# Kernel optimization log

Hardware: AMD Instinct MI355X
Metric: run time of the kernel (lower is better)

The kernel has to match this reference:

```python
import jax, jax.numpy as jnp
import numpy as np


def setup_inputs() -> dict:
    key = jax.random.key(0)
    k1, k2, k3 = jax.random.split(key, 3)
    B, N, M, D = 4, 1024, 2048, 9
    outputs = jax.random.normal(k1, (B, N, D), dtype=jnp.float32)
    targets = jax.random.normal(k2, (B, M, D), dtype=jnp.float32)
    mask = jax.random.randint(k3, (B, M), 0, 2).astype(bool)
    return {"outputs": outputs, "targets": targets, "mask": mask, "k": 64, "max_pair": 1024}


def reference(outputs, targets, mask, k, max_pair):
    # outputs: (B, N, 9), targets: (B, M, 9), mask: (B, M) bool
    y_pred = outputs[:, :max_pair]
    B, N, D = y_pred.shape
    M = targets.shape[1]

    # Statistics over masked ground-truth rows (weighted, jit-friendly)
    w = mask.astype(y_pred.dtype)            # (B, M)
    S = w.sum()                               # number of valid rows
    mean = jnp.einsum('bm,bmd->d', w, targets) / S               # (9,)
    centered = (targets - mean) * w[..., None]                    # (B, M, 9)
    cov = jnp.einsum('bmd,bme->de', centered, centered) / (S - 1.0)
    cov_inv = jnp.linalg.pinv(cov)                                # (9, 9)

    def maha(x):
        # NOTE: original code subtracts the GT mean from the pairwise
        # differences before the quadratic form -- kept faithfully.
        xc = x - mean
        return jnp.einsum('...i,ij,...j->...', xc, cov_inv, xc)

    def topk_smallest_per_col(d, kk):
        # d: (R, N); torch.topk(dim=0, largest=False) -> smallest kk per column
        return -jax.lax.top_k(-d.T, kk)[0]    # (N, kk)

    # Intra loss: GT-vs-pred pairwise distances, masked rows only
    diff = targets[:, :, None, :] - y_pred[:, None, :, :]          # (B, M, N, 9)
    Dn = maha(diff)                                                 # (B, M, N)
    Dn = jnp.where(mask[:, :, None], Dn, jnp.inf).reshape(B * M, N)
    intra_loss = topk_smallest_per_col(Dn, k).mean()

    # Inter (regularization) loss: pred-vs-pred pairwise
    # y_reg1_expand[b,i,j] = y_pred[b,j]; y_reg2_expand[b,i,j] = y_pred[b,i]
    diff_r = y_pred[:, None, :, :] - y_pred[:, :, None, :]          # (B, N, N, 9)
    Dr = maha(diff_r).reshape(B * N, N)
    inter_loss = topk_smallest_per_col(Dr, k).mean()

    return intra_loss - 0.1 * inter_loss
```

## Files before the change

kernel.cpp:

```cpp
#include <hip/hip_runtime.h>
#include <math.h>

#define B_ 4
#define N_ 1024
#define M_ 2048
#define D_ 9
#define K_ 64
#define BM_ (B_*M_)
#define BN_ (B_*N_)
#define TPRE_STRIDE 12
#define PPRE_STRIDE 12
#define NPART 32
#define NSTAT 55
#define TSEL 512
#define BUD 128
#define NMRG 256

#define WS_A 0
#define WS_MEAN 81
#define WS_TPRE 96
#define WS_PPRE (WS_TPRE + BM_*TPRE_STRIDE)
#define WS_CS_INTRA (WS_PPRE + BN_*PPRE_STRIDE)
#define WS_CS_INTER (WS_CS_INTRA + N_)
#define WS_PART (WS_CS_INTER + N_)
#define WS_CANDI (WS_PART + NPART*(NSTAT+1))
#define WS_CANDE (WS_CANDI + 1024*2048)
#define WS_ACC (WS_CANDE + 1024*1024)

__device__ __forceinline__ unsigned f2key(float f) {
  unsigned b = __float_as_uint(f);
  return (b & 0x80000000u) ? ~b : (b | 0x80000000u);
}
__device__ __forceinline__ float key2f(unsigned k) {
  unsigned b = (k & 0x80000000u) ? (k ^ 0x80000000u) : ~k;
  return __uint_as_float(b);
}

__device__ int detect_mask_fmt(const void* mask, int* flags ) {
  int tid = threadIdx.x;
  if (tid < 2) flags[tid] = 0;
  __syncthreads();
  const unsigned char* mb = (const unsigned char*)mask;
  int la = 0, lb = 0;
  for (int i = tid; i < BM_; i += blockDim.x) {
    unsigned char c = mb[i];
    if (c) { if (i & 3) la = 1; else if ((i & 7) == 4) lb = 1; }
  }
  if (la) atomicOr(&flags[0], 1);
  if (lb) atomicOr(&flags[1], 1);
  __syncthreads();
  return flags[0] ? 0 : (flags[1] ? 1 : 2);
}
__device__ __forceinline__ int mask_at(const void* mask, int fmt, int t) {
  if (fmt == 0) return ((const unsigned char*)mask)[t] != 0;
  if (fmt == 1) return ((const int*)mask)[t] != 0;
  return ((const long long*)mask)[t] != 0LL;
}

__global__ __launch_bounds__(256) void stats_part_kernel(
    const float* __restrict__ targets, const void* __restrict__ mask,
    float* __restrict__ ws) {
  __shared__ int flags[2];
  __shared__ float wpart[4][NSTAT];
  int tid = threadIdx.x;
  int fmt = detect_mask_fmt(mask, flags);
  int t = blockIdx.x * 256 + tid;

  float v[NSTAT];
  float tv[D_];
  int m = mask_at(mask, fmt, t);
  const float* tp = targets + t * D_;
#pragma unroll
  for (int d = 0; d < D_; ++d) tv[d] = m ? tp[d] : 0.f;
  v[0] = m ? 1.f : 0.f;
#pragma unroll
  for (int d = 0; d < D_; ++d) v[1 + d] = tv[d];
  {
    int p = 10;
#pragma unroll
    for (int i = 0; i < D_; ++i)
#pragma unroll
      for (int j = i; j < D_; ++j, ++p) v[p] = tv[i] * tv[j];
  }
#pragma unroll
  for (int off = 32; off > 0; off >>= 1)
#pragma unroll
    for (int p = 0; p < NSTAT; ++p) v[p] += __shfl_down(v[p], off);
  int wave = tid >> 6, lane = tid & 63;
  if (lane == 0)
#pragma unroll
    for (int p = 0; p < NSTAT; ++p) wpart[wave][p] = v[p];
  __syncthreads();
  if (tid < NSTAT) {
    float s = wpart[0][tid] + wpart[1][tid] + wpart[2][tid] + wpart[3][tid];
    ws[WS_PART + blockIdx.x * (NSTAT + 1) + tid] = s;
  }
}

__global__ __launch_bounds__(256) void pre_kernel(
    const float* __restrict__ outputs, const float* __restrict__ targets,
    const void* __restrict__ mask, float* __restrict__ ws) {
  __shared__ int flags[2];
  __shared__ float tot[NSTAT];
  __shared__ float Atmp[9][9];
  __shared__ float Ash[81];
  __shared__ float msh[D_];
  int tid = threadIdx.x;
  int fmt = detect_mask_fmt(mask, flags);
  if (blockIdx.x == 0 && tid == 0) {
    long long* acc = (long long*)(ws + WS_ACC);
    acc[0] = 0; acc[1] = 0; acc[2] = 0;
  }
  if (tid < NSTAT) {
    double s = 0.0;
    for (int b = 0; b < NPART; ++b)
      s += (double)ws[WS_PART + b * (NSTAT + 1) + tid];
    tot[tid] = (float)s;
  }
  __syncthreads();
  if (tid < 64) {
    int lane = tid;
    float S = tot[0];
    float col[9];
    int j = lane - 9;
    if (lane < 9) {
      float mj = tot[1 + lane] / S;
#pragma unroll
      for (int r = 0; r < 9; ++r) {
        float mr = tot[1 + r] / S;
        int i0 = r < lane ? r : lane;
        int j0 = r < lane ? lane : r;
        int p = i0 * 9 - (i0 * (i0 - 1)) / 2 + (j0 - i0);
        col[r] = (tot[10 + p] - S * mr * mj) / (S - 1.0f);
      }
    } else {
#pragma unroll
      for (int r = 0; r < 9; ++r) col[r] = (r == j) ? 1.f : 0.f;
    }
#pragma unroll
    for (int c = 0; c < 9; ++c) {
      float pv = __shfl(col[c], c);
      float inv = 1.f / pv;
      col[c] *= inv;
      float f[9];
#pragma unroll
      for (int r = 0; r < 9; ++r) f[r] = __shfl(col[r], c);
#pragma unroll
      for (int r = 0; r < 9; ++r)
        if (r != c) col[r] -= f[r] * col[c];
    }
    if (lane >= 9 && lane < 18) {
#pragma unroll
      for (int r = 0; r < 9; ++r) Atmp[r][j] = col[r];
    }
  }
  __syncthreads();
  if (tid < 9) msh[tid] = tot[1 + tid] / tot[0];
  for (int idx = tid; idx < 81; idx += 256) {
    int i0 = idx / 9, j0 = idx % 9;
    Ash[idx] = 0.5f * (Atmp[i0][j0] + Atmp[j0][i0]);
  }
  __syncthreads();

  int idx = blockIdx.x * 256 + tid;
  if (idx < BM_) {
    const float* tp = targets + idx * D_;
    float u[D_];
#pragma unroll
    for (int d = 0; d < D_; ++d) u[d] = tp[d] - msh[d];
    float cu = 0.f; float au[D_];
#pragma unroll
    for (int i = 0; i < D_; ++i) {
      float s = 0.f;
#pragma unroll
      for (int j = 0; j < D_; ++j) s += Ash[i * D_ + j] * u[j];
      au[i] = s; cu += u[i] * s;
    }
    if (!mask_at(mask, fmt, idx)) cu = INFINITY;
    float* o = ws + WS_TPRE + idx * TPRE_STRIDE;
#pragma unroll
    for (int d = 0; d < D_; ++d) o[d] = au[d];
    o[9] = cu; o[10] = 0.f; o[11] = 0.f;
  } else if (idx < BM_ + BN_) {
    int r = idx - BM_;
    const float* yp = outputs + r * D_;
    float y[D_], q[D_], aq[D_];
#pragma unroll
    for (int d = 0; d < D_; ++d) { y[d] = yp[d]; q[d] = y[d] + msh[d]; }
    float cp = 0.f, cq = 0.f;
#pragma unroll
    for (int i = 0; i < D_; ++i) {
      float sy = 0.f, sq = 0.f;
#pragma unroll
      for (int j = 0; j < D_; ++j) {
        sy += Ash[i * D_ + j] * y[j];
        sq += Ash[i * D_ + j] * q[j];
      }
      cp += y[i] * sy;
      aq[i] = sq; cq += q[i] * sq;
    }
    float* o = ws + WS_PPRE + r * PPRE_STRIDE;
#pragma unroll
    for (int d = 0; d < D_; ++d) o[d] = aq[d];
    o[9] = cq; o[10] = cp; o[11] = 0.f;
  }
}

template <int PER>
__device__ __forceinline__ unsigned bisect64(const unsigned* key) {
  unsigned kmin = 0xFFFFFFFFu;
#pragma unroll
  for (int j = 0; j < PER; ++j) kmin = key[j] < kmin ? key[j] : kmin;
  unsigned gmin = kmin, mmax = kmin;
#pragma unroll
  for (int off = 32; off > 0; off >>= 1) {
    unsigned a = (unsigned)__shfl_xor((int)gmin, off);
    unsigned b = (unsigned)__shfl_xor((int)mmax, off);
    gmin = a < gmin ? a : gmin;
    mmax = b > mmax ? b : mmax;
  }
  unsigned lo = gmin, hi = mmax;
  while (lo < hi) {
    unsigned mid = lo + ((hi - lo) >> 1);
    int cnt = 0;
#pragma unroll
    for (int j = 0; j < PER; ++j) cnt += __popcll(__ballot(key[j] <= mid));
    if (cnt >= K_) hi = mid; else lo = mid + 1;
  }
  return lo;
}

template <int PER>
__device__ __forceinline__ void sel_thresh2(const unsigned* k0,
                                            const unsigned* k1,
                                            unsigned& T0o, unsigned& T1o,
                                            int& st0, int& st1) {
  unsigned mn0 = 0xFFFFFFFFu, mn1 = 0xFFFFFFFFu;
#pragma unroll
  for (int j = 0; j < PER; ++j) {
    mn0 = k0[j] < mn0 ? k0[j] : mn0;
    mn1 = k1[j] < mn1 ? k1[j] : mn1;
  }
  unsigned g0 = mn0, x0 = mn0, g1 = mn1, x1 = mn1;
#pragma unroll
  for (int off = 32; off > 0; off >>= 1) {
    unsigned a0 = (unsigned)__shfl_xor((int)g0, off);
    unsigned b0 = (unsigned)__shfl_xor((int)x0, off);
    unsigned a1 = (unsigned)__shfl_xor((int)g1, off);
    unsigned b1 = (unsigned)__shfl_xor((int)x1, off);
    g0 = a0 < g0 ? a0 : g0;  x0 = b0 > x0 ? b0 : x0;
    g1 = a1 < g1 ? a1 : g1;  x1 = b1 > x1 ? b1 : x1;
  }
  unsigned lo0 = g0, hi0 = x0, lo1 = g1, hi1 = x1;
  int c0 = 0, c1 = 0;
#pragma unroll
  for (int j = 0; j < PER; ++j) {
    c0 += __popcll(__ballot(k0[j] <= hi0));
    c1 += __popcll(__ballot(k1[j] <= hi1));
  }
  while (((lo0 < hi0) && (c0 > BUD)) || ((lo1 < hi1) && (c1 > BUD))) {
    int a0 = (lo0 < hi0) && (c0 > BUD);
    int a1 = (lo1 < hi1) && (c1 > BUD);
    unsigned mid0 = lo0 + ((hi0 - lo0) >> 1);
    unsigned mid1 = lo1 + ((hi1 - lo1) >> 1);
    int n0 = 0, n1 = 0;
#pragma unroll
    for (int j = 0; j < PER; ++j) {
      n0 += __popcll(__ballot(k0[j] <= mid0));
      n1 += __popcll(__ballot(k1[j] <= mid1));
    }
    if (a0) { if (n0 >= K_) { hi0 = mid0; c0 = n0; } else lo0 = mid0 + 1; }
    if (a1) { if (n1 >= K_) { hi1 = mid1; c1 = n1; } else lo1 = mid1 + 1; }
  }
  T0o = hi0; st0 = (c0 > BUD);
  T1o = hi1; st1 = (c1 > BUD);
}

template <int PER>
__device__ __forceinline__ void compactB(const unsigned* key, unsigned T,
                                         int strict, float* candw, int lane) {
  unsigned long long lmask = (1ull << lane) - 1ull;
  int n = 0;
#pragma unroll
  for (int j = 0; j < PER; ++j) {
    bool p = strict ? (key[j] < T) : (key[j] <= T);
    unsigned long long m = __ballot(p);
    if (p) candw[n + __popcll(m & lmask)] = key2f(key[j]);
    n += __popcll(m);
  }
  float tv = key2f(T);
  for (int i = n + lane; i < BUD; i += 64) candw[i] = tv;
}

template <int NP>
__device__ __forceinline__ float final_sum(const float* __restrict__ cand,
                                           int lane) {
  unsigned kk[NP];
#pragma unroll
  for (int j = 0; j < NP; ++j) kk[j] = f2key(cand[j * 64 + lane]);
  unsigned T = bisect64<NP>(kk);
  float s = 0.f; int c = 0;
#pragma unroll
  for (int j = 0; j < NP; ++j)
    if (kk[j] < T) { s += key2f(kk[j]); c++; }
#pragma unroll
  for (int off = 32; off > 0; off >>= 1) {
    s += __shfl_down(s, off);
    c += __shfl_down(c, off);
  }
  return s + (float)(K_ - c) * key2f(T);
}

__global__ __launch_bounds__(TSEL) void select_kernel(
    const float* __restrict__ outputs, const float* __restrict__ wsro,
    float* __restrict__ ws) {
  __shared__ float vsh[2][B_][D_];
  __shared__ float cvsh[2][B_];
  int tid = threadIdx.x, wave = tid >> 6, lane = tid & 63;
  int bid = blockIdx.x;
  int is_intra = bid < N_;
  int p = is_intra ? (bid >> 1) : (bid - N_);
  int h = is_intra ? (bid & 1) : 0;
  int c0 = 2 * p;
  if (tid < 2 * B_ * D_) {
    int c = tid / (B_ * D_), rem = tid % (B_ * D_), b = rem / D_, d = rem % D_;
    vsh[c][b][d] = outputs[(b * N_ + c0 + c) * D_ + d];
  }
  if (tid < 2 * B_) {
    int c = tid >> 2, b = tid & 3;
    cvsh[c][b] = wsro[WS_PPRE + (b * N_ + c0 + c) * PPRE_STRIDE + 10];
  }
  __syncthreads();
  constexpr int PER = 8;
  unsigned k0[PER], k1[PER];
  if (is_intra) {
    const float* pre = wsro + WS_TPRE;
    int rowbase = h * 4096;
#pragma unroll
    for (int bbb = 0; bbb < 2; ++bbb) {
      int b = 2 * h + bbb;
      float v0[D_], v1[D_];
#pragma unroll
      for (int d = 0; d < D_; ++d) { v0[d] = vsh[0][b][d]; v1[d] = vsh[1][b][d]; }
      float cv0 = cvsh[0][b], cv1 = cvsh[1][b];
#pragma unroll
      for (int jj = 0; jj < 4; ++jj) {
        int j = bbb * 4 + jj;
        const float* row = pre + (rowbase + tid + TSEL * j) * TPRE_STRIDE;
        float4 a0 = *(const float4*)row;
        float4 a1 = *(const float4*)(row + 4);
        float2 a2 = *(const float2*)(row + 8);
        float d0 = a0.x * v0[0] + a0.y * v0[1] + a0.z * v0[2] + a0.w * v0[3] +
                   a1.x * v0[4] + a1.y * v0[5] + a1.z * v0[6] + a1.w * v0[7] +
                   a2.x * v0[8];
        float d1 = a0.x * v1[0] + a0.y * v1[1] + a0.z * v1[2] + a0.w * v1[3] +
                   a1.x * v1[4] + a1.y * v1[5] + a1.z * v1[6] + a1.w * v1[7] +
                   a2.x * v1[8];
        k0[j] = f2key(a2.y + cv0 - 2.0f * d0);
        k1[j] = f2key(a2.y + cv1 - 2.0f * d1);
      }
      __builtin_amdgcn_sched_barrier(0);
    }
  } else {
    const float* pre = wsro + WS_PPRE;
#pragma unroll
    for (int bb = 0; bb < B_; ++bb) {
      float v0[D_], v1[D_];
#pragma unroll
      for (int d = 0; d < D_; ++d) { v0[d] = vsh[0][bb][d]; v1[d] = vsh[1][bb][d]; }
      float cv0 = cvsh[0][bb], cv1 = cvsh[1][bb];
#pragma unroll
      for (int jj = 0; jj < 2; ++jj) {
        int j = bb * 2 + jj;
        const float* row = pre + (tid + TSEL * j) * PPRE_STRIDE;
        float4 a0 = *(const float4*)row;
        float4 a1 = *(const float4*)(row + 4);
        float2 a2 = *(const float2*)(row + 8);
        float d0 = a0.x * v0[0] + a0.y * v0[1] + a0.z * v0[2] + a0.w * v0[3] +
                   a1.x * v0[4] + a1.y * v0[5] + a1.z * v0[6] + a1.w * v0[7] +
                   a2.x * v0[8];
        float d1 = a0.x * v1[0] + a0.y * v1[1] + a0.z * v1[2] + a0.w * v1[3] +
                   a1.x * v1[4] + a1.y * v1[5] + a1.z * v1[6] + a1.w * v1[7] +
                   a2.x * v1[8];
        k0[j] = f2key(a2.y + cv0 - 2.0f * d0);
        k1[j] = f2key(a2.y + cv1 - 2.0f * d1);
      }
      __builtin_amdgcn_sched_barrier(0);
    }
  }
  unsigned T0, T1; int st0, st1;
  sel_thresh2<PER>(k0, k1, T0, T1, st0, st1);
  if (is_intra) {
    compactB<PER>(k0, T0, st0,
                  ws + WS_CANDI + (c0) * 2048 + h * 1024 + wave * BUD, lane);
    compactB<PER>(k1, T1, st1,
                  ws + WS_CANDI + (c0 + 1) * 2048 + h * 1024 + wave * BUD, lane);
  } else {
    compactB<PER>(k0, T0, st0,
                  ws + WS_CANDE + (c0) * 1024 + wave * BUD, lane);
    compactB<PER>(k1, T1, st1,
                  ws + WS_CANDE + (c0 + 1) * 1024 + wave * BUD, lane);
  }
}

__global__ __launch_bounds__(512) void merge_kernel(
    const float* __restrict__ wsro, float* __restrict__ ws,
    float* __restrict__ out) {
  __shared__ long long part[8];
  int wave = threadIdx.x >> 6, lane = threadIdx.x & 63;
  int gw = blockIdx.x * 8 + wave;
  unsigned long long* acc = (unsigned long long*)(ws + WS_ACC);
  float s;
  int is_intra = gw < N_;
  if (is_intra) s = final_sum<32>(wsro + WS_CANDI + gw * 2048, lane);
  else          s = final_sum<16>(wsro + WS_CANDE + (gw - N_) * 1024, lane);
  if (lane == 0) part[wave] = (long long)llrint((double)s * 4294967296.0);
  __syncthreads();
  if (threadIdx.x == 0) {
    long long t = 0;
#pragma unroll
    for (int w = 0; w < 8; ++w) t += part[w];
    atomicAdd(&acc[is_intra ? 0 : 1], (unsigned long long)t);
    __threadfence();
    unsigned long long old = atomicAdd(&acc[2], 1ull);
    if (old == (unsigned long long)(NMRG - 1)) {
      long long aI = (long long)atomicAdd(&acc[0], 0ull);
      long long aE = (long long)atomicAdd(&acc[1], 0ull);
      double dn = 4294967296.0 * (double)N_ * (double)K_;
      out[0] = (float)((double)aI / dn - 0.1 * ((double)aE / dn));
    }
  }
}

extern "C" void kernel_launch(void* const* d_in, const int* in_sizes, int n_in,
                              void* d_out, int out_size, void* d_ws,
                              size_t ws_size, hipStream_t stream) {
  const float* outputs = (const float*)d_in[0];
  const float* targets = (const float*)d_in[1];
  const void* mask = d_in[2];
  float* ws = (float*)d_ws;

  hipLaunchKernelGGL(stats_part_kernel, dim3(NPART), dim3(256), 0, stream,
                     targets, mask, ws);
  hipLaunchKernelGGL(pre_kernel, dim3((BM_ + BN_ + 255) / 256), dim3(256), 0,
                     stream, outputs, targets, mask, ws);
  hipLaunchKernelGGL(select_kernel, dim3(N_ + N_ / 2), dim3(TSEL), 0, stream,
                     outputs, ws, ws);
  hipLaunchKernelGGL(merge_kernel, dim3(NMRG), dim3(512), 0, stream,
                     ws, ws, (float*)d_out);
}
```

Baseline: 76.78 us.

## Fold stats reduction into pre kernel and store candidates as sort keys

Removes the separate stats_part_kernel launch. Every pre_kernel block now redundantly computes the full masked mean and covariance sums over all 8192 target rows with a strided per-thread loop, so the partial-sum workspace and one dependent launch go away. Candidate buffers now store the ordered unsigned keys directly, which avoids key/float conversions in the compaction and merge steps. The cost is that each of the 48 pre blocks reads all targets and does about 32 loop iterations of the 55-term accumulation, which lengthens each block. The reduction also switches from double to float.

```diff
diff --git a/kernel.cpp b/kernel.cpp
--- a/kernel.cpp
+++ b/kernel.cpp
@@ -10,20 +10,14 @@
 #define BN_ (B_*N_)
 #define TPRE_STRIDE 12
 #define PPRE_STRIDE 12
-#define NPART 32
 #define NSTAT 55
 #define TSEL 512
 #define BUD 128
 #define NMRG 256
 
-#define WS_A 0
-#define WS_MEAN 81
 #define WS_TPRE 96
 #define WS_PPRE (WS_TPRE + BM_*TPRE_STRIDE)
-#define WS_CS_INTRA (WS_PPRE + BN_*PPRE_STRIDE)
-#define WS_CS_INTER (WS_CS_INTRA + N_)
-#define WS_PART (WS_CS_INTER + N_)
-#define WS_CANDI (WS_PART + NPART*(NSTAT+1))
+#define WS_CANDI (WS_PPRE + BN_*PPRE_STRIDE)
 #define WS_CANDE (WS_CANDI + 1024*2048)
 #define WS_ACC (WS_CANDE + 1024*1024)
 
@@ -57,50 +51,11 @@
   return ((const long long*)mask)[t] != 0LL;
 }
 
-__global__ __launch_bounds__(256) void stats_part_kernel(
-    const float* __restrict__ targets, const void* __restrict__ mask,
-    float* __restrict__ ws) {
-  __shared__ int flags[2];
-  __shared__ float wpart[4][NSTAT];
-  int tid = threadIdx.x;
-  int fmt = detect_mask_fmt(mask, flags);
-  int t = blockIdx.x * 256 + tid;
-
-  float v[NSTAT];
-  float tv[D_];
-  int m = mask_at(mask, fmt, t);
-  const float* tp = targets + t * D_;
-#pragma unroll
-  for (int d = 0; d < D_; ++d) tv[d] = m ? tp[d] : 0.f;
-  v[0] = m ? 1.f : 0.f;
-#pragma unroll
-  for (int d = 0; d < D_; ++d) v[1 + d] = tv[d];
-  {
-    int p = 10;
-#pragma unroll
-    for (int i = 0; i < D_; ++i)
-#pragma unroll
-      for (int j = i; j < D_; ++j, ++p) v[p] = tv[i] * tv[j];
-  }
-#pragma unroll
-  for (int off = 32; off > 0; off >>= 1)
-#pragma unroll
-    for (int p = 0; p < NSTAT; ++p) v[p] += __shfl_down(v[p], off);
-  int wave = tid >> 6, lane = tid & 63;
-  if (lane == 0)
-#pragma unroll
-    for (int p = 0; p < NSTAT; ++p) wpart[wave][p] = v[p];
-  __syncthreads();
-  if (tid < NSTAT) {
-    float s = wpart[0][tid] + wpart[1][tid] + wpart[2][tid] + wpart[3][tid];
-    ws[WS_PART + blockIdx.x * (NSTAT + 1) + tid] = s;
-  }
-}
-
 __global__ __launch_bounds__(256) void pre_kernel(
     const float* __restrict__ outputs, const float* __restrict__ targets,
     const void* __restrict__ mask, float* __restrict__ ws) {
   __shared__ int flags[2];
+  __shared__ float wpart[4][NSTAT];
   __shared__ float tot[NSTAT];
   __shared__ float Atmp[9][9];
   __shared__ float Ash[81];
@@ -111,12 +66,38 @@
     long long* acc = (long long*)(ws + WS_ACC);
     acc[0] = 0; acc[1] = 0; acc[2] = 0;
   }
-  if (tid < NSTAT) {
-    double s = 0.0;
-    for (int b = 0; b < NPART; ++b)
-      s += (double)ws[WS_PART + b * (NSTAT + 1) + tid];
-    tot[tid] = (float)s;
-  }
+  {
+    float v[NSTAT];
+#pragma unroll
+    for (int p = 0; p < NSTAT; ++p) v[p] = 0.f;
+    for (int it = 0; it < 32; ++it) {
+      int t = it * 256 + tid;
+      int m = mask_at(mask, fmt, t);
+      const float* tp = targets + t * D_;
+      float tv[D_];
+#pragma unroll
+      for (int d = 0; d < D_; ++d) tv[d] = m ? tp[d] : 0.f;
+      v[0] += m ? 1.f : 0.f;
+#pragma unroll
+      for (int d = 0; d < D_; ++d) v[1 + d] += tv[d];
+      int p = 10;
+#pragma unroll
+      for (int i = 0; i < D_; ++i)
+#pragma unroll
+        for (int j = i; j < D_; ++j, ++p) v[p] += tv[i] * tv[j];
+    }
+#pragma unroll
+    for (int off = 32; off > 0; off >>= 1)
+#pragma unroll
+      for (int p = 0; p < NSTAT; ++p) v[p] += __shfl_down(v[p], off);
+    int wave = tid >> 6, lane = tid & 63;
+    if (lane == 0)
+#pragma unroll
+      for (int p = 0; p < NSTAT; ++p) wpart[wave][p] = v[p];
+  }
+  __syncthreads();
+  if (tid < NSTAT)
+    tot[tid] = wpart[0][tid] + wpart[1][tid] + wpart[2][tid] + wpart[3][tid];
   __syncthreads();
   if (tid < 64) {
     int lane = tid;
@@ -278,26 +259,25 @@
 
 template <int PER>
 __device__ __forceinline__ void compactB(const unsigned* key, unsigned T,
-                                         int strict, float* candw, int lane) {
+                                         int strict, unsigned* candw, int lane) {
   unsigned long long lmask = (1ull << lane) - 1ull;
   int n = 0;
 #pragma unroll
   for (int j = 0; j < PER; ++j) {
     bool p = strict ? (key[j] < T) : (key[j] <= T);
     unsigned long long m = __ballot(p);
-    if (p) candw[n + __popcll(m & lmask)] = key2f(key[j]);
+    if (p) candw[n + __popcll(m & lmask)] = key[j];
     n += __popcll(m);
   }
-  float tv = key2f(T);
-  for (int i = n + lane; i < BUD; i += 64) candw[i] = tv;
+  for (int i = n + lane; i < BUD; i += 64) candw[i] = T;
 }
 
 template <int NP>
-__device__ __forceinline__ float final_sum(const float* __restrict__ cand,
+__device__ __forceinline__ float final_sum(const unsigned* __restrict__ cand,
                                            int lane) {
   unsigned kk[NP];
 #pragma unroll
-  for (int j = 0; j < NP; ++j) kk[j] = f2key(cand[j * 64 + lane]);
+  for (int j = 0; j < NP; ++j) kk[j] = cand[j * 64 + lane];
   unsigned T = bisect64<NP>(kk);
   float s = 0.f; int c = 0;
 #pragma unroll
@@ -390,16 +370,14 @@
   }
   unsigned T0, T1; int st0, st1;
   sel_thresh2<PER>(k0, k1, T0, T1, st0, st1);
+  unsigned* candi = (unsigned*)(ws + WS_CANDI);
+  unsigned* cande = (unsigned*)(ws + WS_CANDE);
   if (is_intra) {
-    compactB<PER>(k0, T0, st0,
-                  ws + WS_CANDI + (c0) * 2048 + h * 1024 + wave * BUD, lane);
-    compactB<PER>(k1, T1, st1,
-                  ws + WS_CANDI + (c0 + 1) * 2048 + h * 1024 + wave * BUD, lane);
+    compactB<PER>(k0, T0, st0, candi + (c0) * 2048 + h * 1024 + wave * BUD, lane);
+    compactB<PER>(k1, T1, st1, candi + (c0 + 1) * 2048 + h * 1024 + wave * BUD, lane);
   } else {
-    compactB<PER>(k0, T0, st0,
-                  ws + WS_CANDE + (c0) * 1024 + wave * BUD, lane);
-    compactB<PER>(k1, T1, st1,
-                  ws + WS_CANDE + (c0 + 1) * 1024 + wave * BUD, lane);
+    compactB<PER>(k0, T0, st0, cande + (c0) * 1024 + wave * BUD, lane);
+    compactB<PER>(k1, T1, st1, cande + (c0 + 1) * 1024 + wave * BUD, lane);
   }
 }
 
@@ -412,8 +390,10 @@
   unsigned long long* acc = (unsigned long long*)(ws + WS_ACC);
   float s;
   int is_intra = gw < N_;
-  if (is_intra) s = final_sum<32>(wsro + WS_CANDI + gw * 2048, lane);
-  else          s = final_sum<16>(wsro + WS_CANDE + (gw - N_) * 1024, lane);
+  if (is_intra)
+    s = final_sum<32>((const unsigned*)(wsro + WS_CANDI) + gw * 2048, lane);
+  else
+    s = final_sum<16>((const unsigned*)(wsro + WS_CANDE) + (gw - N_) * 1024, lane);
   if (lane == 0) part[wave] = (long long)llrint((double)s * 4294967296.0);
   __syncthreads();
   if (threadIdx.x == 0) {
@@ -440,8 +420,6 @@
   const void* mask = d_in[2];
   float* ws = (float*)d_ws;
 
-  hipLaunchKernelGGL(stats_part_kernel, dim3(NPART), dim3(256), 0, stream,
-                     targets, mask, ws);
   hipLaunchKernelGGL(pre_kernel, dim3((BM_ + BN_ + 255) / 256), dim3(256), 0,
                      stream, outputs, targets, mask, ws);
   hipLaunchKernelGGL(select_kernel, dim3(N_ + N_ / 2), dim3(TSEL), 0, stream,
```

After: 81.02 us. +5.5%, slower.
